# Optimization experiments

Hardware: AMD Instinct MI355X
Metric: run time of the kernel (lower is better)

## Reference

```python
import jax, jax.numpy as jnp
import numpy as np
from jax import lax


def conv2d(x, w, pad=0, b=None):
    out = lax.conv_general_dilated(x, w, (1, 1), [(pad, pad), (pad, pad)],
                                   dimension_numbers=('NCHW', 'OIHW', 'NCHW'))
    if b is not None:
        out = out + b[None, :, None, None]
    return out


def bilinear_resize(x, hw):
    # matches F.interpolate(mode='bilinear', align_corners=False) (half-pixel centers)
    return jax.image.resize(x, x.shape[:2] + tuple(hw), method='bilinear')


def dcn_v2(x, off_feat, w_om, b_om, w, b, dg=8):
    # modulated deformable conv v2, kernel 3x3, stride 1, pad 1, dilation 1
    om = conv2d(off_feat, w_om, pad=1, b=b_om)          # [B, 3*dg*9, H, W]
    B, C, H, W = x.shape
    KK = 9
    Cpg = C // dg
    o1, o2, m = jnp.split(om, 3, axis=1)
    off_y = o1.reshape(B, dg, KK, H, W)
    off_x = o2.reshape(B, dg, KK, H, W)
    mask = jax.nn.sigmoid(m).reshape(B, dg, KK, H, W)
    ks = jnp.arange(3, dtype=x.dtype) - 1.0
    ky = jnp.repeat(ks, 3)   # [9] kernel row offsets
    kx = jnp.tile(ks, 3)     # [9] kernel col offsets
    gy = jnp.arange(H, dtype=x.dtype)
    gx = jnp.arange(W, dtype=x.dtype)
    # sampling coords [B, dg, 9, H, W]
    y = gy[None, None, None, :, None] + ky[None, None, :, None, None] + off_y
    xx = gx[None, None, None, None, :] + kx[None, None, :, None, None] + off_x
    y0 = jnp.floor(y)
    x0 = jnp.floor(xx)
    xg = x.reshape(B, dg, Cpg, H * W)
    val = jnp.zeros((B, dg, Cpg, KK, H, W), x.dtype)
    for dy in (0.0, 1.0):
        for dx in (0.0, 1.0):
            yi = y0 + dy
            xi = x0 + dx
            wgt = (1.0 - jnp.abs(y - yi)) * (1.0 - jnp.abs(xx - xi))
            valid = (yi >= 0) & (yi < H) & (xi >= 0) & (xi < W)  # zero padding outside
            idx = (jnp.clip(yi, 0, H - 1) * W + jnp.clip(xi, 0, W - 1)).astype(jnp.int32)
            idxf = idx.reshape(B, dg, 1, KK * H * W)
            g = jnp.take_along_axis(xg, jnp.broadcast_to(idxf, (B, dg, Cpg, KK * H * W)), axis=3)
            val = val + g.reshape(B, dg, Cpg, KK, H, W) * (wgt * valid)[:, :, None]
    val = val * mask[:, :, None]                         # modulation
    Cout = w.shape[0]
    out = jnp.einsum('bgckhw,ogck->bohw', val, w.reshape(Cout, dg, Cpg, KK))
    return out + b[None, :, None, None]


def sem(x, w_sa, bn_g, bn_b, bn_m, bn_v, w1, gn_g, gn_b):
    # spatial attention
    avg = jnp.mean(x, axis=1, keepdims=True)
    mx = jnp.max(x, axis=1, keepdims=True)
    a = conv2d(jnp.concatenate([avg, mx], axis=1), w_sa, pad=3)
    a = (a - bn_m[None, :, None, None]) * lax.rsqrt(bn_v + 1e-5)[None, :, None, None]
    a = a * bn_g[None, :, None, None] + bn_b[None, :, None, None]
    sa = jax.nn.sigmoid(a)
    x = x + x * sa
    y = conv2d(x, w1)
    # GroupNorm, 32 groups
    B, C, H, W = y.shape
    G = 32
    yr = y.reshape(B, G, C // G, H, W)
    mu = jnp.mean(yr, axis=(2, 3, 4), keepdims=True)
    var = jnp.var(yr, axis=(2, 3, 4), keepdims=True)
    yn = ((yr - mu) * lax.rsqrt(var + 1e-5)).reshape(B, C, H, W)
    return yn * gn_g[None, :, None, None] + gn_b[None, :, None, None]


def setup_inputs() -> dict:
    key = jax.random.key(0)
    ks = jax.random.split(key, 16)
    B, C = 4, 256
    f32 = jnp.float32
    inp = {
        'feat_l': jax.random.normal(ks[0], (B, C, 128, 128), f32),
        'feat_3': jax.random.normal(ks[1], (B, C, 64, 64), f32),
        'feat_4': jax.random.normal(ks[2], (B, C, 32, 32), f32),
        'feat_5': jax.random.normal(ks[3], (B, C, 16, 16), f32),
        'w_off5': jax.random.normal(ks[4], (256, 512, 1, 1), f32) * 0.05,
        'w_om5': jax.random.normal(ks[5], (216, 256, 3, 3), f32) * 0.01,
        'b_om5': jnp.zeros((216,), f32),
        'w_dcn5': jax.random.normal(ks[6], (256, 256, 3, 3), f32) * 0.05,
        'b_dcn5': jnp.zeros((256,), f32),
        'w_c1': jax.random.normal(ks[7], (256, 512, 1, 1), f32) * 0.05,
        'w_off4': jax.random.normal(ks[8], (256, 512, 1, 1), f32) * 0.05,
        'w_om4': jax.random.normal(ks[9], (216, 256, 3, 3), f32) * 0.01,
        'b_om4': jnp.zeros((216,), f32),
        'w_dcn4': jax.random.normal(ks[10], (256, 256, 3, 3), f32) * 0.05,
        'b_dcn4': jnp.zeros((256,), f32),
        'w_sa': jax.random.normal(ks[11], (1, 2, 7, 7), f32) * 0.05,
        'bn_g': jnp.ones((1,), f32),
        'bn_b': jnp.zeros((1,), f32),
        'bn_m': jnp.zeros((1,), f32),
        'bn_v': jnp.ones((1,), f32),
        'w_sem': jax.random.normal(ks[12], (256, 512, 1, 1), f32) * 0.05,
        'gn_g': jnp.ones((256,), f32),
        'gn_b': jnp.zeros((256,), f32),
    }
    return inp


def reference(feat_l, feat_3, feat_4, feat_5,
              w_off5, w_om5, b_om5, w_dcn5, b_dcn5, w_c1,
              w_off4, w_om4, b_om4, w_dcn4, b_dcn4,
              w_sa, bn_g, bn_b, bn_m, bn_v, w_sem, gn_g, gn_b):
    HW4 = feat_4.shape[2:]
    feat_up5 = bilinear_resize(feat_5, HW4)
    off5 = conv2d(jnp.concatenate([feat_4, feat_up5 * 2.0], axis=1), w_off5)
    feat_5_align = jax.nn.relu(dcn_v2(feat_up5, off5, w_om5, b_om5, w_dcn5, b_dcn5))
    feat_4 = conv2d(jnp.concatenate([feat_5_align, feat_4], axis=1), w_c1)
    HW3 = feat_3.shape[2:]
    feat_up4 = bilinear_resize(feat_4, HW3)
    off4 = conv2d(jnp.concatenate([feat_3, feat_up4 * 2.0], axis=1), w_off4)
    feat_4_align = jax.nn.relu(dcn_v2(feat_up4, off4, w_om4, b_om4, w_dcn4, b_dcn4))
    feat_3 = jnp.concatenate([feat_4_align, feat_3], axis=1)
    HW2 = feat_l.shape[2:]
    feat_2 = bilinear_resize(feat_3, HW2)
    return sem(feat_2, w_sa, bn_g, bn_b, bn_m, bn_v, w_sem, gn_g, gn_b)
```

## Files before the change

### kernel.cpp

```cpp
#include <hip/hip_runtime.h>
#include <math.h>


typedef _Float16 h_t;
typedef _Float16 h2 __attribute__((ext_vector_type(2)));
typedef _Float16 h4 __attribute__((ext_vector_type(4)));
typedef _Float16 h8 __attribute__((ext_vector_type(8)));
typedef float f4 __attribute__((ext_vector_type(4)));

static inline int cdiv(long long a, long long b) { return (int)((a + b - 1) / b); }

template <int PERM>
__global__ void prep_w_kernel(const float* __restrict__ W, h_t* __restrict__ Wp,
                              int M, int K) {
  long long idx = (long long)blockIdx.x * 256 + threadIdx.x;
  if (idx >= 512LL * K) return;
  int within = (int)(idx & 4095);
  int m = within >> 5, k = within & 31;
  long long t2 = idx >> 12;
  int s = (int)(t2 & 1);
  long long t3 = t2 >> 1;
  int nck = K >> 5;
  int c = (int)(t3 % nck), mblk = (int)(t3 / nck);
  int gm = mblk * 128 + m, gk = c * 32 + k;
  if (PERM) gk = (gk & 255) * 9 + (gk >> 8);
  float f = (gm < M) ? W[(long long)gm * K + gk] : 0.f;
  h_t hi = (h_t)f;
  Wp[idx] = s ? (h_t)(f - (float)hi) : hi;
}

template <int LOGOW>
__global__ void upsample2x_q_kernel(const float* __restrict__ in, float* __restrict__ out,
                                    int NQ) {
  const int OW = 1 << LOGOW, OHW = OW * OW, IW = OW >> 1;
  long long idx = (long long)blockIdx.x * 256 + threadIdx.x;
  if (idx >= (long long)NQ * OHW) return;
  int p = (int)(idx & (OHW - 1));
  int q = (int)(idx >> (2 * LOGOW));
  int oh = p >> LOGOW, ow = p & (OW - 1);
  int iy = oh >> 1, ix = ow >> 1;
  int iy2 = (oh & 1) ? min(iy + 1, IW - 1) : max(iy - 1, 0);
  int ix2 = (ow & 1) ? min(ix + 1, IW - 1) : max(ix - 1, 0);
  const float* pb = in + (long long)q * 4 * IW * IW;
  f4 o;
#pragma unroll
  for (int j = 0; j < 4; ++j) {
    const float* pc = pb + (long long)j * IW * IW;
    o[j] = 0.5625f * pc[iy * IW + ix] + 0.1875f * (pc[iy * IW + ix2] + pc[iy2 * IW + ix])
         + 0.0625f * pc[iy2 * IW + ix2];
  }
  *(f4*)(out + idx * 4) = o;
}

template <typename TA>
__global__ void concat_h_kernel(const TA* __restrict__ A, const float* __restrict__ Bp,
                                h_t* __restrict__ out, int C1, int C2, int HW, float scale) {
  long long idx = (long long)blockIdx.x * blockDim.x + threadIdx.x;
  long long total = 4LL * (C1 + C2) * HW;
  if (idx >= total) return;
  int p = (int)(idx % HW);
  long long t = idx / HW;
  int c = (int)(t % (C1 + C2));
  int b = (int)(t / (C1 + C2));
  float v;
  if (c < C1) v = (float)A[((long long)b * C1 + c) * HW + p];
  else        v = scale * Bp[((long long)b * C2 + (c - C1)) * HW + p];
  out[idx] = (h_t)v;
}

template <typename TA>
__global__ void concat_a_kernel(const TA* __restrict__ A, h_t* __restrict__ out,
                                int C1, int Ctot, int HW) {
  long long idx = (long long)blockIdx.x * 256 + threadIdx.x;
  long long total = 4LL * C1 * HW;
  if (idx >= total) return;
  int p = (int)(idx % HW);
  long long t = idx / HW;
  int c = (int)(t % C1);
  int b = (int)(t / C1);
  out[((long long)b * Ctot + c) * HW + p] = (h_t)(float)A[((long long)b * C1 + c) * HW + p];
}

__global__ void concat_bq_kernel(const float* __restrict__ xq, h_t* __restrict__ out,
                                 int C1, int C2, int HW, float scale) {
  long long idx = (long long)blockIdx.x * 256 + threadIdx.x;
  long long total = 4LL * (C2 >> 2) * HW;
  if (idx >= total) return;
  int p = (int)(idx % HW);
  long long t = idx / HW;
  int q = (int)(t % (C2 >> 2));
  int b = (int)(t / (C2 >> 2));
  f4 v = *(const f4*)(xq + ((long long)(b * (C2 >> 2) + q) * HW + p) * 4);
  h_t* ob = out + ((long long)b * (C1 + C2) + C1 + q * 4) * HW + p;
  ob[0]            = (h_t)(scale * v.x);
  ob[(long long)HW]     = (h_t)(scale * v.y);
  ob[(long long)2 * HW] = (h_t)(scale * v.z);
  ob[(long long)3 * HW] = (h_t)(scale * v.w);
}

template <int RELU, int OUTH, int TWO>
__global__ __launch_bounds__(256) void mgemm_kernel(
    const h_t* __restrict__ Wp, const h_t* __restrict__ B, void* __restrict__ Cv,
    const float* __restrict__ bias, int Mstore, int N, int K,
    long long sB, long long sC) {
  __shared__ __align__(16) h_t Ah[128 * 40];
  __shared__ __align__(16) h_t Al[TWO ? 128 * 40 : 8];
  __shared__ __align__(16) h_t Bs[64 * 40];
  const int tid = threadIdx.x;
  const int bn = blockIdx.x * 64;
  const int mblk = blockIdx.y;
  const int z = blockIdx.z;
  const h_t* Bb = B + (long long)z * sB;
  const int nck = K >> 5;
  const h_t* Wt = Wp + (long long)mblk * nck * 8192 +
                  (TWO ? (tid << 5) : ((tid >> 1) << 5) + ((tid & 1) << 4));
  const int wid = tid >> 6, lane = tid & 63;
  const int wm = (wid >> 1) * 64, wn = (wid & 1) * 32;
  const int l15 = lane & 15, q = lane >> 4;
  f4 acc[4][2] = {};
  h_t* Adst = TWO ? (tid >= 128 ? Al : Ah) + (tid & 127) * 40
                  : Ah + (tid >> 1) * 40 + ((tid & 1) << 4);
  const int kp = tid >> 4, ngf = tid & 15;
  h_t* Bdst = Bs + ngf * 4 * 40 + kp * 2;
  for (int c = 0; c < nck; ++c) {
    const h_t* asrc = Wt + c * 8192;
    if (TWO) {
#pragma unroll
      for (int i = 0; i < 4; ++i)
        *(h8*)(Adst + i * 8) = *(const h8*)(asrc + i * 8);
    } else {
      *(h8*)(Adst) = *(const h8*)(asrc);
      *(h8*)(Adst + 8) = *(const h8*)(asrc + 8);
    }
    const h_t* bsrc = Bb + (long long)(c * 32 + kp * 2) * N + bn + ngf * 4;
    h4 r0 = *(const h4*)bsrc;
    h4 r1 = *(const h4*)(bsrc + N);
#pragma unroll
    for (int j = 0; j < 4; ++j) {
      h2 v; v.x = r0[j]; v.y = r1[j];
      *(h2*)(Bdst + j * 40) = v;
    }
    __syncthreads();
    h8 bf[2];
#pragma unroll
    for (int nt = 0; nt < 2; ++nt)
      bf[nt] = *(const h8*)(Bs + (wn + nt * 16 + l15) * 40 + q * 8);
#pragma unroll
    for (int mt = 0; mt < 4; ++mt) {
      const int ro = (wm + mt * 16 + l15) * 40 + q * 8;
      h8 ahi = *(const h8*)(Ah + ro);
#pragma unroll
      for (int nt = 0; nt < 2; ++nt)
        acc[mt][nt] = __builtin_amdgcn_mfma_f32_16x16x32_f16(ahi, bf[nt], acc[mt][nt], 0, 0, 0);
      if (TWO) {
        h8 alo = *(const h8*)(Al + ro);
#pragma unroll
        for (int nt = 0; nt < 2; ++nt)
          acc[mt][nt] = __builtin_amdgcn_mfma_f32_16x16x32_f16(alo, bf[nt], acc[mt][nt], 0, 0, 0);
      }
    }
    __syncthreads();
  }
#pragma unroll
  for (int mt = 0; mt < 4; ++mt)
#pragma unroll
    for (int nt = 0; nt < 2; ++nt) {
      int n = bn + wn + nt * 16 + l15;
#pragma unroll
      for (int r = 0; r < 4; ++r) {
        int row = mblk * 128 + wm + mt * 16 + q * 4 + r;
        if (row < Mstore) {
          float v = acc[mt][nt][r] + (bias ? bias[row] : 0.f);
          if (RELU) v = fmaxf(v, 0.f);
          if (OUTH) ((h_t*)Cv)[(long long)z * sC + (long long)row * N + n] = (h_t)v;
          else      ((float*)Cv)[(long long)z * sC + (long long)row * N + n] = v;
        }
      }
    }
}

template <int LOGW>
__global__ __launch_bounds__(256) void mconv_kernel(
    const h_t* __restrict__ Wp, const h_t* __restrict__ Off, float* __restrict__ Cf,
    const float* __restrict__ bias, int HW) {
  const int W = 1 << LOGW, H = HW >> LOGW;
  __shared__ __align__(16) h_t Ah[128 * 40];
  __shared__ __align__(16) h_t Bs[64 * 40];
  const int tid = threadIdx.x;
  const int p0 = blockIdx.x * 64;
  const int mblk = blockIdx.y;
  const int z = blockIdx.z;
  const h_t* Ob = Off + (long long)z * 256 * HW;
  const h_t* Wt = Wp + (long long)mblk * 72 * 8192 + ((tid >> 1) << 5) + ((tid & 1) << 4);
  const int wid = tid >> 6, lane = tid & 63;
  const int wm = (wid >> 1) * 64, wn = (wid & 1) * 32;
  const int l15 = lane & 15, q = lane >> 4;
  f4 acc[4][2] = {};
  h_t* Adst = Ah + (tid >> 1) * 40 + ((tid & 1) << 4);
  const int kp = tid >> 4, ngf = tid & 15;
  h_t* Bdst = Bs + ngf * 4 * 40 + kp * 2;
  int py[4], px[4];
#pragma unroll
  for (int j = 0; j < 4; ++j) {
    int p = p0 + ngf * 4 + j;
    py[j] = p >> LOGW;
    px[j] = p & (W - 1);
  }
  for (int tap = 0; tap < 9; ++tap) {
    const int dy = tap / 3 - 1, dx = tap - (tap / 3) * 3 - 1;
#pragma unroll 1
    for (int c2 = 0; c2 < 8; ++c2) {
      const int c = tap * 8 + c2;
      const h_t* asrc = Wt + c * 8192;
      *(h8*)(Adst) = *(const h8*)(asrc);
      *(h8*)(Adst + 8) = *(const h8*)(asrc + 8);
      h_t tmp[2][4];
#pragma unroll
      for (int kk = 0; kk < 2; ++kk) {
        const h_t* src = Ob + (long long)(c2 * 32 + kp * 2 + kk) * HW;
#pragma unroll
        for (int j = 0; j < 4; ++j) {
          int sy = py[j] + dy, sx = px[j] + dx;
          h_t v = (h_t)0.f;
          if (sy >= 0 && sy < H && sx >= 0 && sx < W) v = src[sy * W + sx];
          tmp[kk][j] = v;
        }
      }
#pragma unroll
      for (int j = 0; j < 4; ++j) {
        h2 v; v.x = tmp[0][j]; v.y = tmp[1][j];
        *(h2*)(Bdst + j * 40) = v;
      }
      __syncthreads();
      h8 bf[2];
#pragma unroll
      for (int nt = 0; nt < 2; ++nt)
        bf[nt] = *(const h8*)(Bs + (wn + nt * 16 + l15) * 40 + q * 8);
#pragma unroll
      for (int mt = 0; mt < 4; ++mt) {
        const int ro = (wm + mt * 16 + l15) * 40 + q * 8;
        h8 ahi = *(const h8*)(Ah + ro);
#pragma unroll
        for (int nt = 0; nt < 2; ++nt)
          acc[mt][nt] = __builtin_amdgcn_mfma_f32_16x16x32_f16(ahi, bf[nt], acc[mt][nt], 0, 0, 0);
      }
      __syncthreads();
    }
  }
  float* Cb = Cf + (long long)z * 216 * HW;
#pragma unroll
  for (int mt = 0; mt < 4; ++mt)
#pragma unroll
    for (int nt = 0; nt < 2; ++nt) {
      int n = p0 + wn + nt * 16 + l15;
#pragma unroll
      for (int r = 0; r < 4; ++r) {
        int row = mblk * 128 + wm + mt * 16 + q * 4 + r;
        if (row < 216)
          Cb[(long long)row * HW + n] = acc[mt][nt][r] + bias[row];
      }
    }
}

template <int LOGW>
__global__ __launch_bounds__(256) void dcn_col_kernel(
    const float* __restrict__ x, const float* __restrict__ om,
    h_t* __restrict__ col, int b0) {
  const int W = 1 << LOGW, H = W, HW = W * W;
  int p = blockIdx.x * 256 + threadIdx.x;
  int gk = blockIdx.y;
  int g = gk / 9, k9 = gk - g * 9;
  int bz = blockIdx.z;
  int b = b0 + bz;
  int h = p >> LOGW, wc = p & (W - 1);
  const float* omb = om + (long long)b * 216 * HW;
  float offy = omb[(long long)gk * HW + p];
  float offx = omb[(long long)(72 + gk) * HW + p];
  float mraw = omb[(long long)(144 + gk) * HW + p];
  float mask = 1.f / (1.f + expf(-mraw));
  float y = (float)h + (float)(k9 / 3 - 1) + offy;
  float xx = (float)wc + (float)(k9 % 3 - 1) + offx;
  float y0f = floorf(y), x0f = floorf(xx);
  int y0 = (int)y0f, x0 = (int)x0f;
  float fy = y - y0f, fx = xx - x0f;
  float w00 = (1.f - fy) * (1.f - fx), w01 = (1.f - fy) * fx;
  float w10 = fy * (1.f - fx), w11 = fy * fx;
  bool iy0 = (y0 >= 0) & (y0 < H), iy1 = (y0 + 1 >= 0) & (y0 + 1 < H);
  bool ix0 = (x0 >= 0) & (x0 < W), ix1 = (x0 + 1 >= 0) & (x0 + 1 < W);
  w00 = (iy0 & ix0) ? w00 : 0.f;
  w01 = (iy0 & ix1) ? w01 : 0.f;
  w10 = (iy1 & ix0) ? w10 : 0.f;
  w11 = (iy1 & ix1) ? w11 : 0.f;
  int y0c = min(max(y0, 0), H - 1), y1c = min(max(y0 + 1, 0), H - 1);
  int x0c = min(max(x0, 0), W - 1), x1c = min(max(x0 + 1, 0), W - 1);
  int i00 = y0c * W + x0c, i01 = y0c * W + x1c, i10 = y1c * W + x0c, i11 = y1c * W + x1c;
  const float* xb = x + ((long long)b * 256 + g * 32) * HW;
  h_t* cb = col + ((long long)bz * 2304 + (long long)(g * 32) * 9 + k9) * HW + p;
#pragma unroll 1
  for (int qd = 0; qd < 8; qd += 2) {
    f4 a00[2], a01[2], a10[2], a11[2];
#pragma unroll
    for (int u = 0; u < 2; ++u) {
      const float* xq = xb + (long long)(qd + u) * HW * 4;
      a00[u] = *(const f4*)(xq + i00 * 4);
      a01[u] = *(const f4*)(xq + i01 * 4);
      a10[u] = *(const f4*)(xq + i10 * 4);
      a11[u] = *(const f4*)(xq + i11 * 4);
    }
#pragma unroll
    for (int u = 0; u < 2; ++u)
#pragma unroll
      for (int j = 0; j < 4; ++j) {
        float v = w00 * a00[u][j] + w01 * a01[u][j] + w10 * a10[u][j] + w11 * a11[u][j];
        cb[(long long)((qd + u) * 4 + j) * 9 * HW] = (h_t)(v * mask);
      }
  }
}

__global__ void avgmax_kernel(const h_t* __restrict__ f3c, float* __restrict__ am) {
  int tid = threadIdx.x;
  int P = blockIdx.x * 64 + (tid >> 2);
  int cq = tid & 3;
  int b = P >> 14, p = P & 16383;
  int oh = p >> 7, ow = p & 127;
  int iy = oh >> 1, ix = ow >> 1;
  int iy2 = (oh & 1) ? min(iy + 1, 63) : max(iy - 1, 0);
  int ix2 = (ow & 1) ? min(ix + 1, 63) : max(ix - 1, 0);
  int i00 = iy * 64 + ix, i01 = iy * 64 + ix2, i10 = iy2 * 64 + ix, i11 = iy2 * 64 + ix2;
  const h_t* base = f3c + (long long)b * 512 * 4096 + (long long)cq * 4096;
  float sum = 0.f, mx = -3.4e38f;
  for (int c = 0; c < 128; c++) {
    const h_t* pc = base + (long long)c * 4 * 4096;
    float v = 0.5625f * (float)pc[i00] + 0.1875f * ((float)pc[i01] + (float)pc[i10])
            + 0.0625f * (float)pc[i11];
    sum += v;
    mx = fmaxf(mx, v);
  }
  sum += __shfl_xor(sum, 1); sum += __shfl_xor(sum, 2);
  mx = fmaxf(mx, __shfl_xor(mx, 1)); mx = fmaxf(mx, __shfl_xor(mx, 2));
  if (cq == 0) {
    am[(long long)b * 2 * 16384 + p] = sum * (1.f / 512.f);
    am[(long long)b * 2 * 16384 + 16384 + p] = mx;
  }
}

__global__ void sa_kernel(const float* __restrict__ am, const float* __restrict__ w_sa,
                          const float* __restrict__ bn_g, const float* __restrict__ bn_b,
                          const float* __restrict__ bn_m, const float* __restrict__ bn_v,
                          float* __restrict__ sa) {
  int idx = blockIdx.x * 64 + threadIdx.x;
  int b = idx >> 14, p = idx & 16383;
  int oh = p >> 7, ow = p & 127;
  float acc = 0.f;
  for (int ci = 0; ci < 2; ci++) {
    const float* base = am + ((long long)b * 2 + ci) * 16384;
    for (int dy = 0; dy < 7; dy++) {
      int yy = oh + dy - 3;
      if (yy < 0 || yy > 127) continue;
      for (int dx = 0; dx < 7; dx++) {
        int xx = ow + dx - 3;
        if (xx < 0 || xx > 127) continue;
        acc += w_sa[ci * 49 + dy * 7 + dx] * base[yy * 128 + xx];
      }
    }
  }
  float a = (acc - bn_m[0]) * rsqrtf(bn_v[0] + 1e-5f);
  a = a * bn_g[0] + bn_b[0];
  sa[idx] = 1.f / (1.f + expf(-a));
}

__global__ __launch_bounds__(256) void gn_partials_kernel(
    const float* __restrict__ z, const float* __restrict__ sa,
    float2* __restrict__ partials) {
  long long idx = (long long)blockIdx.x * 256 + threadIdx.x;
  int ow = (int)(idx & 127);
  long long t = idx >> 7;
  int oh = (int)(t & 127);
  t >>= 7;
  int c = (int)(t & 255);
  int b = (int)(t >> 8);
  int iy = oh >> 1, ix = ow >> 1;
  int iy2 = (oh & 1) ? min(iy + 1, 63) : max(iy - 1, 0);
  int ix2 = (ow & 1) ? min(ix + 1, 63) : max(ix - 1, 0);
  const float* zp = z + (long long)(b * 256 + c) * 4096;
  float v = 0.5625f * zp[iy * 64 + ix] + 0.1875f * (zp[iy * 64 + ix2] + zp[iy2 * 64 + ix])
          + 0.0625f * zp[iy2 * 64 + ix2];
  float s = sa[((long long)b << 14) + (oh << 7) + ow];
  float y = v * (1.f + s);
  float ps = y, pss = y * y;
#pragma unroll
  for (int off = 32; off > 0; off >>= 1) {
    ps += __shfl_down(ps, off);
    pss += __shfl_down(pss, off);
  }
  __shared__ float rs[2][4];
  int lane = threadIdx.x & 63, wv = threadIdx.x >> 6;
  if (lane == 0) { rs[0][wv] = ps; rs[1][wv] = pss; }
  __syncthreads();
  if (threadIdx.x == 0) {
    float2 pr;
    pr.x = rs[0][0] + rs[0][1] + rs[0][2] + rs[0][3];
    pr.y = rs[1][0] + rs[1][1] + rs[1][2] + rs[1][3];
    partials[blockIdx.x] = pr;
  }
}

__global__ __launch_bounds__(256) void gn_reduce_kernel(const float2* __restrict__ partials,
                                                        float* __restrict__ stats) {
  int bg = blockIdx.x;
  int b = bg >> 5, g = bg & 31;
  int base = b * 16384 + g * 512;
  float2 p0 = partials[base + threadIdx.x];
  float2 p1 = partials[base + 256 + threadIdx.x];
  float s = p0.x + p1.x, ss = p0.y + p1.y;
#pragma unroll
  for (int off = 32; off > 0; off >>= 1) {
    s += __shfl_down(s, off);
    ss += __shfl_down(ss, off);
  }
  __shared__ float rs[2][4];
  int lane = threadIdx.x & 63, wv = threadIdx.x >> 6;
  if (lane == 0) { rs[0][wv] = s; rs[1][wv] = ss; }
  __syncthreads();
  if (threadIdx.x == 0) {
    float S = rs[0][0] + rs[0][1] + rs[0][2] + rs[0][3];
    float SS = rs[1][0] + rs[1][1] + rs[1][2] + rs[1][3];
    float n = 8.f * 16384.f;
    float mu = S / n;
    float var = SS / n - mu * mu;
    stats[bg * 2] = mu;
    stats[bg * 2 + 1] = rsqrtf(var + 1e-5f);
  }
}

__global__ __launch_bounds__(256) void gn_apply_fused_kernel(
    const float* __restrict__ z, const float* __restrict__ sa,
    const float* __restrict__ stats, const float* __restrict__ gg,
    const float* __restrict__ gb, float* __restrict__ out) {
  long long i4 = (long long)blockIdx.x * 256 + threadIdx.x;
  long long e = i4 << 2;
  int ow0 = (int)(e & 127);
  int oh = (int)((e >> 7) & 127);
  int c = (int)((e >> 14) & 255);
  int b = (int)(e >> 22);
  int bg = b * 32 + (c >> 3);
  float mu = stats[bg * 2], rstd = stats[bg * 2 + 1];
  float sc = rstd * gg[c];
  float sh = gb[c] - mu * sc;
  int iy = oh >> 1;
  int iy2 = (oh & 1) ? min(iy + 1, 63) : max(iy - 1, 0);
  const float* zp = z + (long long)(b * 256 + c) * 4096;
  f4 sv = *(const f4*)(sa + (((long long)b << 14) + (oh << 7) + ow0));
  f4 o;
#pragma unroll
  for (int j = 0; j < 4; ++j) {
    int ow = ow0 + j;
    int ix = ow >> 1;
    int ix2 = (ow & 1) ? min(ix + 1, 63) : max(ix - 1, 0);
    float v = 0.5625f * zp[iy * 64 + ix] + 0.1875f * (zp[iy * 64 + ix2] + zp[iy2 * 64 + ix])
            + 0.0625f * zp[iy2 * 64 + ix2];
    float y = v * (1.f + sv[j]);
    o[j] = y * sc + sh;
  }
  *(f4*)(out + e) = o;
}


extern "C" void kernel_launch(void* const* d_in, const int* in_sizes, int n_in,
                              void* d_out, int out_size, void* d_ws, size_t ws_size,
                              hipStream_t stream) {
  const float* feat_3 = (const float*)d_in[1];
  const float* feat_4 = (const float*)d_in[2];
  const float* feat_5 = (const float*)d_in[3];
  const float* w_off5 = (const float*)d_in[4];
  const float* w_om5  = (const float*)d_in[5];
  const float* b_om5  = (const float*)d_in[6];
  const float* w_dcn5 = (const float*)d_in[7];
  const float* b_dcn5 = (const float*)d_in[8];
  const float* w_c1   = (const float*)d_in[9];
  const float* w_off4 = (const float*)d_in[10];
  const float* w_om4  = (const float*)d_in[11];
  const float* b_om4  = (const float*)d_in[12];
  const float* w_dcn4 = (const float*)d_in[13];
  const float* b_dcn4 = (const float*)d_in[14];
  const float* w_sa   = (const float*)d_in[15];
  const float* bn_g   = (const float*)d_in[16];
  const float* bn_b   = (const float*)d_in[17];
  const float* bn_m   = (const float*)d_in[18];
  const float* bn_v   = (const float*)d_in[19];
  const float* w_sem  = (const float*)d_in[20];
  const float* gn_g   = (const float*)d_in[21];
  const float* gn_b   = (const float*)d_in[22];
  float* out = (float*)d_out;
  float* ws = (float*)d_ws;

  const long long o_Wp    = 0;
  const long long o_up5   = o_Wp + 2883584;
  const long long o_off5h = o_up5 + 1048576;
  const long long o_om5   = o_off5h + 524288;
  const long long o_a5    = o_om5 + 884736;
  const long long o_f4n   = o_a5 + 1048576;
  const long long o_up4   = o_f4n + 1048576;
  const long long o_off4h = o_up4 + 4194304;
  const long long o_om4   = o_off4h + 2097152;
  const long long o_sh    = o_om4 + 3538944;

  const long long shAll = 18874368;
  bool allb = ws_size >= (size_t)(o_sh + shAll) * 4;

  h_t* WpH = (h_t*)ws;
  h_t* wp_off5 = WpH;
  h_t* wp_dcn5 = wp_off5 + 262144;
  h_t* wp_c1   = wp_dcn5 + 1179648;
  h_t* wp_om5  = wp_c1 + 262144;
  h_t* wp_off4 = wp_om5 + 1179648;
  h_t* wp_dcn4 = wp_off4 + 262144;
  h_t* wp_om4  = wp_dcn4 + 1179648;
  h_t* wp_sem  = wp_om4 + 1179648;

  float* up5   = ws + o_up5;
  h_t*   off5h = (h_t*)(ws + o_off5h);
  float* om5   = ws + o_om5;
  float* a5    = ws + o_a5;
  float* f4n   = ws + o_f4n;
  float* up4   = ws + o_up4;
  h_t*   off4h = (h_t*)(ws + o_off4h);
  float* om4   = ws + o_om4;
  h_t*   shH   = (h_t*)(ws + o_sh);
  h_t*   f4aH  = off4h;
  float* z64   = up4;
  float* am    = up5;
  float* sa    = am + 131072;
  float* gnst  = sa + 65536;
  float2* gnpart = (float2*)(gnst + 256);

  dim3 blk(256);

  prep_w_kernel<0><<<cdiv(512LL * 512, 256), blk, 0, stream>>>(w_off5, wp_off5, 256, 512);
  prep_w_kernel<0><<<cdiv(512LL * 2304, 256), blk, 0, stream>>>(w_dcn5, wp_dcn5, 256, 2304);
  prep_w_kernel<0><<<cdiv(512LL * 512, 256), blk, 0, stream>>>(w_c1, wp_c1, 256, 512);
  prep_w_kernel<1><<<cdiv(512LL * 2304, 256), blk, 0, stream>>>(w_om5, wp_om5, 216, 2304);
  prep_w_kernel<0><<<cdiv(512LL * 512, 256), blk, 0, stream>>>(w_off4, wp_off4, 256, 512);
  prep_w_kernel<0><<<cdiv(512LL * 2304, 256), blk, 0, stream>>>(w_dcn4, wp_dcn4, 256, 2304);
  prep_w_kernel<1><<<cdiv(512LL * 2304, 256), blk, 0, stream>>>(w_om4, wp_om4, 216, 2304);
  prep_w_kernel<0><<<cdiv(512LL * 512, 256), blk, 0, stream>>>(w_sem, wp_sem, 256, 512);

  upsample2x_q_kernel<5><<<1024, blk, 0, stream>>>(feat_5, up5, 256);
  concat_a_kernel<float><<<cdiv(4LL * 256 * 1024, 256), blk, 0, stream>>>(
      feat_4, shH, 256, 512, 1024);
  concat_bq_kernel<<<cdiv(4LL * 64 * 1024, 256), blk, 0, stream>>>(
      up5, shH, 256, 256, 1024, 2.f);
  mgemm_kernel<0, 1, 0><<<dim3(16, 2, 4), blk, 0, stream>>>(
      wp_off5, shH, off5h, nullptr, 256, 1024, 512, 512LL * 1024, 256LL * 1024);
  mconv_kernel<5><<<dim3(16, 2, 4), blk, 0, stream>>>(wp_om5, off5h, om5, b_om5, 1024);
  dcn_col_kernel<5><<<dim3(4, 72, 4), blk, 0, stream>>>(up5, om5, shH, 0);
  mgemm_kernel<1, 0, 1><<<dim3(16, 2, 4), blk, 0, stream>>>(
      wp_dcn5, shH, a5, b_dcn5, 256, 1024, 2304, 2304LL * 1024, 256LL * 1024);
  concat_h_kernel<float><<<cdiv(4LL * 512 * 1024, 256), blk, 0, stream>>>(
      a5, feat_4, shH, 256, 256, 1024, 1.f);
  mgemm_kernel<0, 0, 1><<<dim3(16, 2, 4), blk, 0, stream>>>(
      wp_c1, shH, f4n, nullptr, 256, 1024, 512, 512LL * 1024, 256LL * 1024);

  upsample2x_q_kernel<6><<<4096, blk, 0, stream>>>(f4n, up4, 256);
  concat_a_kernel<float><<<cdiv(4LL * 256 * 4096, 256), blk, 0, stream>>>(
      feat_3, shH, 256, 512, 4096);
  concat_bq_kernel<<<cdiv(4LL * 64 * 4096, 256), blk, 0, stream>>>(
      up4, shH, 256, 256, 4096, 2.f);
  mgemm_kernel<0, 1, 0><<<dim3(64, 2, 4), blk, 0, stream>>>(
      wp_off4, shH, off4h, nullptr, 256, 4096, 512, 512LL * 4096, 256LL * 4096);
  mconv_kernel<6><<<dim3(64, 2, 4), blk, 0, stream>>>(wp_om4, off4h, om4, b_om4, 4096);
  if (allb) {
    dcn_col_kernel<6><<<dim3(16, 72, 4), blk, 0, stream>>>(up4, om4, shH, 0);
    mgemm_kernel<1, 1, 1><<<dim3(64, 2, 4), blk, 0, stream>>>(
        wp_dcn4, shH, f4aH, b_dcn4, 256, 4096, 2304, 2304LL * 4096, 256LL * 4096);
  } else {
    for (int b = 0; b < 4; b++) {
      dcn_col_kernel<6><<<dim3(16, 72, 1), blk, 0, stream>>>(up4, om4, shH, b);
      mgemm_kernel<1, 1, 1><<<dim3(64, 2, 1), blk, 0, stream>>>(
          wp_dcn4, shH, f4aH + (long long)b * 1048576, b_dcn4, 256, 4096, 2304, 0, 0);
    }
  }
  concat_h_kernel<h_t><<<cdiv(4LL * 512 * 4096, 256), blk, 0, stream>>>(
      f4aH, feat_3, shH, 256, 256, 4096, 1.f);

  avgmax_kernel<<<1024, blk, 0, stream>>>(shH, am);
  sa_kernel<<<1024, dim3(64), 0, stream>>>(am, w_sa, bn_g, bn_b, bn_m, bn_v, sa);
  mgemm_kernel<0, 0, 1><<<dim3(64, 2, 4), blk, 0, stream>>>(
      wp_sem, shH, z64, nullptr, 256, 4096, 512, 512LL * 4096, 256LL * 4096);
  gn_partials_kernel<<<65536, blk, 0, stream>>>(z64, sa, gnpart);
  gn_reduce_kernel<<<128, blk, 0, stream>>>(gnpart, gnst);
  gn_apply_fused_kernel<<<16384, blk, 0, stream>>>(z64, sa, gnst, gn_g, gn_b, out);
}
```

Baseline: 810.2 us.

## Store offset features pixel-major and load mconv operands directly without LDS

The offset GEMM now writes its fp16 output transposed (pixel-major, 256 channels contiguous) with 4-wide vector stores. The 3x3 offset/mask conv kernel then reads B fragments straight from global memory as 8-half vectors and loads the pre-packed weight fragments directly, dropping the shared-memory staging and both barriers per k-chunk. This removes scattered scalar gathers and sync overhead, but every wave now reads global/L2 directly with some redundant traffic and less latency hiding.

```diff
diff --git a/kernel.cpp b/kernel.cpp
--- a/kernel.cpp
+++ b/kernel.cpp
@@ -166,14 +166,28 @@
 #pragma unroll
     for (int nt = 0; nt < 2; ++nt) {
       int n = bn + wn + nt * 16 + l15;
-#pragma unroll
-      for (int r = 0; r < 4; ++r) {
-        int row = mblk * 128 + wm + mt * 16 + q * 4 + r;
-        if (row < Mstore) {
-          float v = acc[mt][nt][r] + (bias ? bias[row] : 0.f);
-          if (RELU) v = fmaxf(v, 0.f);
-          if (OUTH) ((h_t*)Cv)[(long long)z * sC + (long long)row * N + n] = (h_t)v;
-          else      ((float*)Cv)[(long long)z * sC + (long long)row * N + n] = v;
+      if (OUTH == 2) {
+        int row0 = mblk * 128 + wm + mt * 16 + q * 4;
+        if (row0 + 3 < Mstore) {
+          h4 hv;
+#pragma unroll
+          for (int r = 0; r < 4; ++r) {
+            float v = acc[mt][nt][r] + (bias ? bias[row0 + r] : 0.f);
+            if (RELU) v = fmaxf(v, 0.f);
+            hv[r] = (h_t)v;
+          }
+          *(h4*)((h_t*)Cv + (long long)z * sC + (long long)n * 256 + row0) = hv;
+        }
+      } else {
+#pragma unroll
+        for (int r = 0; r < 4; ++r) {
+          int row = mblk * 128 + wm + mt * 16 + q * 4 + r;
+          if (row < Mstore) {
+            float v = acc[mt][nt][r] + (bias ? bias[row] : 0.f);
+            if (RELU) v = fmaxf(v, 0.f);
+            if (OUTH) ((h_t*)Cv)[(long long)z * sC + (long long)row * N + n] = (h_t)v;
+            else      ((float*)Cv)[(long long)z * sC + (long long)row * N + n] = v;
+          }
         }
       }
     }
@@ -181,70 +195,56 @@
 
 template <int LOGW>
 __global__ __launch_bounds__(256) void mconv_kernel(
-    const h_t* __restrict__ Wp, const h_t* __restrict__ Off, float* __restrict__ Cf,
+    const h_t* __restrict__ Wp, const h_t* __restrict__ OffT, float* __restrict__ Cf,
     const float* __restrict__ bias, int HW) {
   const int W = 1 << LOGW, H = HW >> LOGW;
-  __shared__ __align__(16) h_t Ah[128 * 40];
-  __shared__ __align__(16) h_t Bs[64 * 40];
   const int tid = threadIdx.x;
   const int p0 = blockIdx.x * 64;
   const int mblk = blockIdx.y;
   const int z = blockIdx.z;
-  const h_t* Ob = Off + (long long)z * 256 * HW;
-  const h_t* Wt = Wp + (long long)mblk * 72 * 8192 + ((tid >> 1) << 5) + ((tid & 1) << 4);
+  const h_t* Ot = OffT + (long long)z * HW * 256;
+  const h_t* Wb = Wp + (long long)mblk * 72 * 8192;
   const int wid = tid >> 6, lane = tid & 63;
   const int wm = (wid >> 1) * 64, wn = (wid & 1) * 32;
   const int l15 = lane & 15, q = lane >> 4;
+  const int aoff = (wm + l15) * 32 + q * 8;
   f4 acc[4][2] = {};
-  h_t* Adst = Ah + (tid >> 1) * 40 + ((tid & 1) << 4);
-  const int kp = tid >> 4, ngf = tid & 15;
-  h_t* Bdst = Bs + ngf * 4 * 40 + kp * 2;
-  int py[4], px[4];
-#pragma unroll
-  for (int j = 0; j < 4; ++j) {
-    int p = p0 + ngf * 4 + j;
-    py[j] = p >> LOGW;
-    px[j] = p & (W - 1);
+  int py[2], px[2];
+#pragma unroll
+  for (int nt = 0; nt < 2; ++nt) {
+    int p = p0 + wn + nt * 16 + l15;
+    py[nt] = p >> LOGW;
+    px[nt] = p & (W - 1);
   }
   for (int tap = 0; tap < 9; ++tap) {
     const int dy = tap / 3 - 1, dx = tap - (tap / 3) * 3 - 1;
-#pragma unroll 1
+    const h_t* bsrc[2];
+    bool bok[2];
+#pragma unroll
+    for (int nt = 0; nt < 2; ++nt) {
+      int sy = py[nt] + dy, sx = px[nt] + dx;
+      bok[nt] = (sy >= 0) & (sy < H) & (sx >= 0) & (sx < W);
+      int sp = bok[nt] ? (sy * W + sx) : 0;
+      bsrc[nt] = Ot + (long long)sp * 256 + q * 8;
+    }
+#pragma unroll 2
     for (int c2 = 0; c2 < 8; ++c2) {
       const int c = tap * 8 + c2;
-      const h_t* asrc = Wt + c * 8192;
-      *(h8*)(Adst) = *(const h8*)(asrc);
-      *(h8*)(Adst + 8) = *(const h8*)(asrc + 8);
-      h_t tmp[2][4];
-#pragma unroll
-      for (int kk = 0; kk < 2; ++kk) {
-        const h_t* src = Ob + (long long)(c2 * 32 + kp * 2 + kk) * HW;
-#pragma unroll
-        for (int j = 0; j < 4; ++j) {
-          int sy = py[j] + dy, sx = px[j] + dx;
-          h_t v = (h_t)0.f;
-          if (sy >= 0 && sy < H && sx >= 0 && sx < W) v = src[sy * W + sx];
-          tmp[kk][j] = v;
-        }
-      }
-#pragma unroll
-      for (int j = 0; j < 4; ++j) {
-        h2 v; v.x = tmp[0][j]; v.y = tmp[1][j];
-        *(h2*)(Bdst + j * 40) = v;
-      }
-      __syncthreads();
       h8 bf[2];
 #pragma unroll
-      for (int nt = 0; nt < 2; ++nt)
-        bf[nt] = *(const h8*)(Bs + (wn + nt * 16 + l15) * 40 + q * 8);
+      for (int nt = 0; nt < 2; ++nt) {
+        h8 v = {};
+        if (bok[nt]) v = *(const h8*)(bsrc[nt] + c2 * 32);
+        bf[nt] = v;
+      }
+      const h_t* aw = Wb + (long long)c * 8192 + aoff;
 #pragma unroll
       for (int mt = 0; mt < 4; ++mt) {
-        const int ro = (wm + mt * 16 + l15) * 40 + q * 8;
-        h8 ahi = *(const h8*)(Ah + ro);
+        h8 af = *(const h8*)(aw + mt * 512);
 #pragma unroll
         for (int nt = 0; nt < 2; ++nt)
-          acc[mt][nt] = __builtin_amdgcn_mfma_f32_16x16x32_f16(ahi, bf[nt], acc[mt][nt], 0, 0, 0);
-      }
-      __syncthreads();
+          acc[mt][nt] = __builtin_amdgcn_mfma_f32_16x16x32_f16(af, bf[nt], acc[mt][nt], 0, 0, 0);
+      }
     }
   }
   float* Cb = Cf + (long long)z * 216 * HW;
@@ -550,7 +550,7 @@
       feat_4, shH, 256, 512, 1024);
   concat_bq_kernel<<<cdiv(4LL * 64 * 1024, 256), blk, 0, stream>>>(
       up5, shH, 256, 256, 1024, 2.f);
-  mgemm_kernel<0, 1, 0><<<dim3(16, 2, 4), blk, 0, stream>>>(
+  mgemm_kernel<0, 2, 0><<<dim3(16, 2, 4), blk, 0, stream>>>(
       wp_off5, shH, off5h, nullptr, 256, 1024, 512, 512LL * 1024, 256LL * 1024);
   mconv_kernel<5><<<dim3(16, 2, 4), blk, 0, stream>>>(wp_om5, off5h, om5, b_om5, 1024);
   dcn_col_kernel<5><<<dim3(4, 72, 4), blk, 0, stream>>>(up5, om5, shH, 0);
@@ -566,7 +566,7 @@
       feat_3, shH, 256, 512, 4096);
   concat_bq_kernel<<<cdiv(4LL * 64 * 4096, 256), blk, 0, stream>>>(
       up4, shH, 256, 256, 4096, 2.f);
-  mgemm_kernel<0, 1, 0><<<dim3(64, 2, 4), blk, 0, stream>>>(
+  mgemm_kernel<0, 2, 0><<<dim3(64, 2, 4), blk, 0, stream>>>(
       wp_off4, shH, off4h, nullptr, 256, 4096, 512, 512LL * 4096, 256LL * 4096);
   mconv_kernel<6><<<dim3(64, 2, 4), blk, 0, stream>>>(wp_om4, off4h, om4, b_om4, 4096);
   if (allb) {
```

After: 772.6 us. -4.6%, faster.
